# Performance work log

Measured on AMD Instinct MI355X. Metric: run time of the kernel, lower is better.

The kernel has to match this reference:

```python
import jax, jax.numpy as jnp
import numpy as np

COMMITMENT_COST = 0.25


def setup_inputs() -> dict:
    key = jax.random.key(0)
    k1, k2 = jax.random.split(key)
    B, H, W, D, K = 64, 32, 32, 64, 1024
    x = jax.random.normal(k1, (B, H, W, D), dtype=jnp.float32)
    # variance_scaling(fan_in=D, uniform) ~ U(-sqrt(3/D), sqrt(3/D)); plain normal*scale is fine for a reference
    embeddings = jax.random.uniform(k2, (D, K), dtype=jnp.float32,
                                    minval=-np.sqrt(3.0 / D), maxval=np.sqrt(3.0 / D))
    return {"x": x, "embeddings": embeddings}


def reference(x, embeddings):
    D = embeddings.shape[0]
    K = embeddings.shape[1]
    flat = x.reshape(-1, D)                                   # [N, D]
    # squared euclidean distance: ||f||^2 - 2 f.E + ||e||^2 -> [N, K]
    distance = (jnp.sum(flat ** 2, axis=1, keepdims=True)
                - 2.0 * jnp.matmul(flat, embeddings)
                + jnp.sum(embeddings ** 2, axis=0, keepdims=True))
    encoding_indices_flat = jnp.argmax(-distance, axis=1)     # [N]
    encodings = jax.nn.one_hot(encoding_indices_flat, K, dtype=distance.dtype)  # [N, K]
    encoding_indices = encoding_indices_flat.reshape(x.shape[:-1])
    # quantize: gather rows of E^T -> same shape as x
    quantized = jnp.take(embeddings.T, encoding_indices, axis=0)
    e_latent_loss = jnp.mean((jax.lax.stop_gradient(quantized) - x) ** 2)
    q_latent_loss = jnp.mean((quantized - jax.lax.stop_gradient(x)) ** 2)
    loss = q_latent_loss + COMMITMENT_COST * e_latent_loss
    quantized_st = x + jax.lax.stop_gradient(quantized - x)   # straight-through
    avg_probs = jnp.mean(encodings, axis=0)                   # [K]
    perplexity = jnp.exp(-jnp.sum(avg_probs * jnp.log(avg_probs + 1e-10)))
    return quantized_st, loss, perplexity, encoding_indices
```

## Files before the change

### kernel.cpp

```cpp
#include <hip/hip_runtime.h>
#include <math.h>


typedef __attribute__((ext_vector_type(8))) short short8v;
typedef __attribute__((ext_vector_type(4))) float float4v;
typedef unsigned short u16;
typedef unsigned int u32;

constexpr int D = 64;
constexpr int K = 1024;
constexpr int NPTS = 65536;
constexpr long QOFF = (long)NPTS * D;
constexpr float BIAS = 24.0f;
constexpr float GATE = 5e-3f;

constexpr size_t OFF_LOSS = 0;
constexpr size_t OFF_CNT  = 256;
constexpr size_t OFF_EC   = OFF_CNT + 4096;
constexpr size_t OFF_ECB  = OFF_EC + 4096;
constexpr size_t OFF_ET   = OFF_ECB + 4096;
constexpr size_t OFF_STG  = OFF_ET + (size_t)K * D * 4;

__device__ __forceinline__ float med3(float a, float b, float c) {
  return __builtin_amdgcn_fmed3f(a, b, c);
}
__device__ __forceinline__ u16 bf16rtn(float x) {
  u32 u = __float_as_uint(x);
  return (u16)((u + 0x7fffu + ((u >> 16) & 1u)) >> 16);
}
__device__ __forceinline__ float bf2f(u16 h) {
  return __uint_as_float(((u32)h) << 16);
}
__device__ __forceinline__ void gl_lds16(const void* g, void* l) {
  __builtin_amdgcn_global_load_lds(
      (const __attribute__((address_space(1))) u32*)g,
      (__attribute__((address_space(3))) u32*)l, 16, 0, 0);
}

__global__ __launch_bounds__(256) void vq_prep(const float* __restrict__ E,
                                               float* __restrict__ eC,
                                               float* __restrict__ eCb,
                                               float* __restrict__ Et,
                                               unsigned char* __restrict__ stg,
                                               double* __restrict__ lossSum,
                                               int* __restrict__ counts) {
  const int b = blockIdx.x;
  const int tid = threadIdx.x;
  if (b < 32) {
    int gid = b * 256 + tid;
    int k = gid & 1023;
    int g = gid >> 10;
    float v[8];
#pragma unroll
    for (int j = 0; j < 8; ++j) v[j] = E[(g * 8 + j) * K + k];
    *(float4*)&Et[(size_t)k * 64 + g * 8] = make_float4(v[0], v[1], v[2], v[3]);
    *(float4*)&Et[(size_t)k * 64 + g * 8 + 4] = make_float4(v[4], v[5], v[6], v[7]);
    short8v hv, lv;
#pragma unroll
    for (int j = 0; j < 8; ++j) {
      float m2 = -2.0f * v[j];
      u16 h = bf16rtn(m2);
      hv[j] = (short)h;
      lv[j] = (short)bf16rtn(m2 - bf2f(h));
    }
    size_t rowb = (size_t)(k >> 7) * 32768 + (size_t)(k & 127) * 256;
    int s = g >> 2, q = g & 3;
    int off = (s * 64 + q * 16) ^ ((k & 7) * 16);
    *(short8v*)&stg[rowb + off] = hv;
    *(short8v*)&stg[rowb + 128 + off] = lv;
  } else {
    int k = (b - 32) * 256 + tid;
    float c = __fmul_rn(E[k], E[k]);
#pragma unroll
    for (int d = 1; d < D; ++d) {
      float vv = E[d * K + k];
      c = __fadd_rn(c, __fmul_rn(vv, vv));
    }
    eC[k] = c;
    eCb[k] = c + BIAS;
    counts[k] = 0;
    if (k == 0) *lossSum = 0.0;
  }
}

__global__ __launch_bounds__(256) void vq_main(const float* __restrict__ x,
                                               const unsigned char* __restrict__ stg,
                                               const float* __restrict__ eC,
                                               const float* __restrict__ eCb,
                                               const float* __restrict__ Etg,
                                               float* __restrict__ out,
                                               double* __restrict__ lossSum,
                                               int* __restrict__ counts) {
  __shared__ __align__(16) unsigned char sbuf[4][2][8192];
  __shared__ __align__(16) float ecb[1024];
  __shared__ __align__(16) float topbuf[256 * 4];
  __shared__ int bkbuf[128];

  const int tid = threadIdx.x;
  const int w = tid >> 6;
  const int lane = tid & 63;
  const int col = lane & 15;
  const int quad = lane >> 4;
  const int blockBase = blockIdx.x * 128;
  const float INF = __builtin_inff();

  *(float4*)&ecb[tid * 4] = *(const float4*)&eCb[tid * 4];

  short8v Bh[2][2], Bl[2][2];
#pragma unroll
  for (int pt = 0; pt < 2; ++pt) {
    const float* xp = x + (size_t)(blockBase + w * 32 + pt * 16 + col) * 64;
#pragma unroll
    for (int s = 0; s < 2; ++s) {
      const float4* src = (const float4*)(xp + s * 32 + quad * 8);
      float4 a = src[0], b = src[1];
      float xs[8] = {a.x, a.y, a.z, a.w, b.x, b.y, b.z, b.w};
      short8v hf, lf;
#pragma unroll
      for (int j = 0; j < 8; ++j) {
        u16 h = bf16rtn(xs[j]);
        hf[j] = (short)h;
        lf[j] = (short)bf16rtn(xs[j] - bf2f(h));
      }
      Bh[pt][s] = hf;
      Bl[pt][s] = lf;
    }
  }

  {
    const unsigned char* s0 = stg + (size_t)lane * 16;
#pragma unroll
    for (int i = 0; i < 8; ++i)
      gl_lds16(s0 + i * 1024, &sbuf[w][0][i * 1024 + lane * 16]);
#pragma unroll
    for (int i = 0; i < 8; ++i)
      gl_lds16(s0 + 8192 + i * 1024, &sbuf[w][1][i * 1024 + lane * 16]);
  }
  asm volatile("s_waitcnt lgkmcnt(0)" ::: "memory");
  __builtin_amdgcn_s_barrier();
  __builtin_amdgcn_sched_barrier(0);
  asm volatile("" ::: "memory");

  float b1[2] = {INF, INF}, b2[2] = {INF, INF};
  const int swz = (col & 7) * 16;

#pragma unroll 1
  for (int ch = 0; ch < 32; ++ch) {
    const unsigned char* bufB = sbuf[w][ch & 1];
    if (ch < 31) {
      asm volatile("s_waitcnt vmcnt(8)" ::: "memory");
    } else {
      asm volatile("s_waitcnt vmcnt(0)" ::: "memory");
    }
#pragma unroll
    for (int ct2 = 0; ct2 < 2; ++ct2) {
      const int rb = ct2 * 4096 + col * 256;
      short8v Ah0 = *(const short8v*)&bufB[rb + ((quad * 16) ^ swz)];
      short8v Ah1 = *(const short8v*)&bufB[rb + ((64 + quad * 16) ^ swz)];
      short8v Al0 = *(const short8v*)&bufB[rb + 128 + ((quad * 16) ^ swz)];
      short8v Al1 = *(const short8v*)&bufB[rb + 128 + ((64 + quad * 16) ^ swz)];
      float4v Ci = *(const float4v*)&ecb[ch * 32 + ct2 * 16 + quad * 4];
#pragma unroll
      for (int pt = 0; pt < 2; ++pt) {
        float4v Ca = Ci;
        float4v Cb = {0.f, 0.f, 0.f, 0.f};
        Ca = __builtin_amdgcn_mfma_f32_16x16x32_bf16(Ah0, Bh[pt][0], Ca, 0, 0, 0);
        Cb = __builtin_amdgcn_mfma_f32_16x16x32_bf16(Ah1, Bh[pt][1], Cb, 0, 0, 0);
        Ca = __builtin_amdgcn_mfma_f32_16x16x32_bf16(Al0, Bh[pt][0], Ca, 0, 0, 0);
        Cb = __builtin_amdgcn_mfma_f32_16x16x32_bf16(Al1, Bh[pt][1], Cb, 0, 0, 0);
        Ca = __builtin_amdgcn_mfma_f32_16x16x32_bf16(Ah0, Bl[pt][0], Ca, 0, 0, 0);
        Cb = __builtin_amdgcn_mfma_f32_16x16x32_bf16(Ah1, Bl[pt][1], Cb, 0, 0, 0);
#pragma unroll
        for (int r = 0; r < 4; ++r) {
          float dv = Ca[r] + Cb[r];
          u32 u = (__float_as_uint(dv) & 0xffffff00u) |
                  (u32)(ch * 8 + ct2 * 4 + r);
          float v = __uint_as_float(u);
          float pb = b1[pt];
          b1[pt] = fminf(pb, v);
          b2[pt] = med3(pb, b2[pt], v);
        }
      }
    }
    asm volatile("s_waitcnt lgkmcnt(0)" ::: "memory");
    if (ch < 30) {
      const unsigned char* s2 = stg + (size_t)(ch + 2) * 8192 + (size_t)lane * 16;
#pragma unroll
      for (int i = 0; i < 8; ++i)
        gl_lds16(s2 + i * 1024, &sbuf[w][ch & 1][i * 1024 + lane * 16]);
    }
  }

  topbuf[tid * 4 + 0] = b1[0];
  topbuf[tid * 4 + 1] = b2[0];
  topbuf[tid * 4 + 2] = b1[1];
  topbuf[tid * 4 + 3] = b2[1];
  __syncthreads();

  if (tid < 128) {
    const int mw = tid >> 5, mpt = (tid >> 4) & 1, mcol = tid & 15;
    float cv[8];
    int cq[8];
    float mv0 = INF, mv1 = INF;
    int q0 = 0;
#pragma unroll
    for (int q = 0; q < 4; ++q) {
      int lbase = (mw * 64 + q * 16 + mcol) * 4 + mpt * 2;
#pragma unroll
      for (int j = 0; j < 2; ++j) {
        float v = topbuf[lbase + j];
        cv[q * 2 + j] = v;
        cq[q * 2 + j] = q;
        if (v < mv0) { mv1 = mv0; mv0 = v; q0 = q; }
        else if (v < mv1) { mv1 = v; }
      }
    }
    u32 lb = __float_as_uint(mv0) & 255u;
    int bestk = (int)((lb >> 3) * 32 + ((lb >> 2) & 1) * 16 + q0 * 4 + (lb & 3));

    if (mv1 - mv0 < GATE) {
      const float* f = x + (size_t)(blockBase + tid) * 64;
      float r8[8];
#pragma unroll
      for (int j = 0; j < 8; ++j) { float fv = f[j]; r8[j] = __fmul_rn(fv, fv); }
#pragma unroll
      for (int i = 8; i < D; i += 8)
#pragma unroll
        for (int j = 0; j < 8; ++j) {
          float fv = f[i + j];
          r8[j] = __fadd_rn(r8[j], __fmul_rn(fv, fv));
        }
      float A = __fadd_rn(__fadd_rn(__fadd_rn(r8[0], r8[1]), __fadd_rn(r8[2], r8[3])),
                          __fadd_rn(__fadd_rn(r8[4], r8[5]), __fadd_rn(r8[6], r8[7])));
      float bd = INF;
      int bkk = K;
#pragma unroll
      for (int c = 0; c < 8; ++c) {
        u32 cb = __float_as_uint(cv[c]) & 255u;
        int k = (int)((cb >> 3) * 32 + ((cb >> 2) & 1) * 16 + cq[c] * 4 + (cb & 3));
        const float* er = Etg + (size_t)k * 64;
        float m = 0.f;
#pragma unroll
        for (int d = 0; d < D; ++d) m = __fmaf_rn(f[d], er[d], m);
        float dist = __fadd_rn(__fsub_rn(A, __fmul_rn(2.f, m)), eC[k]);
        bool better = (dist < bd) || (dist == bd && k < bkk);
        bd = better ? dist : bd;
        bkk = better ? k : bkk;
      }
      bestk = bkk;
    }

    bkbuf[tid] = bestk;
    out[QOFF + 2 + blockBase + tid] = (float)bestk;
    atomicAdd(&counts[bestk], 1);
  }
  __syncthreads();

  const int pp = tid >> 1, half = tid & 1;
  const int bk = bkbuf[pp];
  const float4* et = (const float4*)(Etg + (size_t)bk * 64 + half * 32);
  const float4* xr = (const float4*)(x + (size_t)(blockBase + pp) * 64 + half * 32);
  float4* ov = (float4*)(out + (size_t)(blockBase + pp) * 64 + half * 32);
  float errs = 0.f;
#pragma unroll
  for (int i = 0; i < 8; ++i) {
    float4 qv = et[i];
    float4 xv = xr[i];
    float dx;
    dx = qv.x - xv.x; errs = fmaf(dx, dx, errs);
    dx = qv.y - xv.y; errs = fmaf(dx, dx, errs);
    dx = qv.z - xv.z; errs = fmaf(dx, dx, errs);
    dx = qv.w - xv.w; errs = fmaf(dx, dx, errs);
    ov[i] = qv;
  }
  double de = (double)errs;
#pragma unroll
  for (int off = 32; off > 0; off >>= 1) de += __shfl_down(de, off, 64);
  if (lane == 0) atomicAdd(lossSum, de);
}

__global__ __launch_bounds__(256) void vq_finalize(const double* __restrict__ lossSum,
                                                   const int* __restrict__ counts,
                                                   float* __restrict__ out) {
  __shared__ double sh[256];
  double ent = 0.0;
  for (int k = threadIdx.x; k < K; k += 256) {
    double pp = (double)counts[k] / (double)NPTS;
    ent += pp * log(pp + 1e-10);
  }
  sh[threadIdx.x] = ent;
  __syncthreads();
  for (int s = 128; s > 0; s >>= 1) {
    if (threadIdx.x < s) sh[threadIdx.x] += sh[threadIdx.x + s];
    __syncthreads();
  }
  if (threadIdx.x == 0) {
    out[QOFF + 0] = (float)(1.25 * (*lossSum) / (double)((long)NPTS * D));
    out[QOFF + 1] = (float)exp(-sh[0]);
  }
}

extern "C" void kernel_launch(void* const* d_in, const int* in_sizes, int n_in,
                              void* d_out, int out_size, void* d_ws, size_t ws_size,
                              hipStream_t stream) {
  const float* x = (const float*)d_in[0];
  const float* E = (const float*)d_in[1];
  float* out = (float*)d_out;

  char* ws = (char*)d_ws;
  double* lossSum = (double*)(ws + OFF_LOSS);
  int* counts = (int*)(ws + OFF_CNT);
  float* eC = (float*)(ws + OFF_EC);
  float* eCb = (float*)(ws + OFF_ECB);
  float* Etg = (float*)(ws + OFF_ET);
  unsigned char* stgb = (unsigned char*)(ws + OFF_STG);

  vq_prep<<<36, 256, 0, stream>>>(E, eC, eCb, Etg, stgb, lossSum, counts);
  vq_main<<<NPTS / 128, 256, 0, stream>>>(x, stgb, eC, eCb, Etg, out,
                                          lossSum, counts);
  vq_finalize<<<1, 256, 0, stream>>>(lossSum, counts, out);
}
```

Measured before the change: 129.4 us.

## Split codebook across waves instead of points, reduce top-2 via shuffles

Each wave now handles all 128 points of the block against a quarter of the codebook (256 codes), not 32 points against all 1024 codes. Each wave streams only its own 8 chunks of staged codebook, and the staging layout is reorganised into MFMA-fragment order so LDS reads are contiguous and unswizzled. The cross-lane top-2 merge now uses xor shuffles and writes into the reused stage buffer, which drops the separate topbuf. In exchange each thread holds 8 point fragments (Bh/Bl[8][2]) and 16 top-2 accumulators, which raises register pressure, and the initial barrier before the loop is removed.

New measurement: 144.5 us. 11.7% more time.

```diff
diff --git a/kernel.cpp b/kernel.cpp
--- a/kernel.cpp
+++ b/kernel.cpp
@@ -63,11 +63,11 @@
       hv[j] = (short)h;
       lv[j] = (short)bf16rtn(m2 - bf2f(h));
     }
-    size_t rowb = (size_t)(k >> 7) * 32768 + (size_t)(k & 127) * 256;
     int s = g >> 2, q = g & 3;
-    int off = (s * 64 + q * 16) ^ ((k & 7) * 16);
-    *(short8v*)&stg[rowb + off] = hv;
-    *(short8v*)&stg[rowb + 128 + off] = lv;
+    size_t tb = (size_t)(k >> 4) * 4096;
+    int lanoff = (q * 16 + (k & 15)) * 16;
+    *(short8v*)&stg[tb + (size_t)s * 1024 + lanoff] = hv;
+    *(short8v*)&stg[tb + (size_t)(2 + s) * 1024 + lanoff] = lv;
   } else {
     int k = (b - 32) * 256 + tid;
     float c = __fmul_rn(E[k], E[k]);
@@ -93,7 +93,6 @@
                                                int* __restrict__ counts) {
   __shared__ __align__(16) unsigned char sbuf[4][2][8192];
   __shared__ __align__(16) float ecb[1024];
-  __shared__ __align__(16) float topbuf[256 * 4];
   __shared__ int bkbuf[128];
 
   const int tid = threadIdx.x;
@@ -106,10 +105,10 @@
 
   *(float4*)&ecb[tid * 4] = *(const float4*)&eCb[tid * 4];
 
-  short8v Bh[2][2], Bl[2][2];
-#pragma unroll
-  for (int pt = 0; pt < 2; ++pt) {
-    const float* xp = x + (size_t)(blockBase + w * 32 + pt * 16 + col) * 64;
+  short8v Bh[8][2], Bl[8][2];
+#pragma unroll
+  for (int pt = 0; pt < 8; ++pt) {
+    const float* xp = x + (size_t)(blockBase + pt * 16 + col) * 64;
 #pragma unroll
     for (int s = 0; s < 2; ++s) {
       const float4* src = (const float4*)(xp + s * 32 + quad * 8);
@@ -128,7 +127,7 @@
   }
 
   {
-    const unsigned char* s0 = stg + (size_t)lane * 16;
+    const unsigned char* s0 = stg + (size_t)(w * 8) * 8192 + (size_t)lane * 16;
 #pragma unroll
     for (int i = 0; i < 8; ++i)
       gl_lds16(s0 + i * 1024, &sbuf[w][0][i * 1024 + lane * 16]);
@@ -136,32 +135,29 @@
     for (int i = 0; i < 8; ++i)
       gl_lds16(s0 + 8192 + i * 1024, &sbuf[w][1][i * 1024 + lane * 16]);
   }
-  asm volatile("s_waitcnt lgkmcnt(0)" ::: "memory");
-  __builtin_amdgcn_s_barrier();
-  __builtin_amdgcn_sched_barrier(0);
-  asm volatile("" ::: "memory");
-
-  float b1[2] = {INF, INF}, b2[2] = {INF, INF};
-  const int swz = (col & 7) * 16;
+
+  float b1[8] = {INF, INF, INF, INF, INF, INF, INF, INF};
+  float b2[8] = {INF, INF, INF, INF, INF, INF, INF, INF};
 
 #pragma unroll 1
-  for (int ch = 0; ch < 32; ++ch) {
+  for (int ch = 0; ch < 8; ++ch) {
     const unsigned char* bufB = sbuf[w][ch & 1];
-    if (ch < 31) {
+    if (ch < 7) {
       asm volatile("s_waitcnt vmcnt(8)" ::: "memory");
     } else {
       asm volatile("s_waitcnt vmcnt(0)" ::: "memory");
     }
 #pragma unroll
     for (int ct2 = 0; ct2 < 2; ++ct2) {
-      const int rb = ct2 * 4096 + col * 256;
-      short8v Ah0 = *(const short8v*)&bufB[rb + ((quad * 16) ^ swz)];
-      short8v Ah1 = *(const short8v*)&bufB[rb + ((64 + quad * 16) ^ swz)];
-      short8v Al0 = *(const short8v*)&bufB[rb + 128 + ((quad * 16) ^ swz)];
-      short8v Al1 = *(const short8v*)&bufB[rb + 128 + ((64 + quad * 16) ^ swz)];
-      float4v Ci = *(const float4v*)&ecb[ch * 32 + ct2 * 16 + quad * 4];
-#pragma unroll
-      for (int pt = 0; pt < 2; ++pt) {
+      const unsigned char* fb = bufB + ct2 * 4096 + lane * 16;
+      short8v Ah0 = *(const short8v*)(fb);
+      short8v Ah1 = *(const short8v*)(fb + 1024);
+      short8v Al0 = *(const short8v*)(fb + 2048);
+      short8v Al1 = *(const short8v*)(fb + 3072);
+      float4v Ci = *(const float4v*)&ecb[w * 256 + ch * 32 + ct2 * 16 + quad * 4];
+      const int idb = ch * 32 + ct2 * 16 + quad * 4;
+#pragma unroll
+      for (int pt = 0; pt < 8; ++pt) {
         float4v Ca = Ci;
         float4v Cb = {0.f, 0.f, 0.f, 0.f};
         Ca = __builtin_amdgcn_mfma_f32_16x16x32_bf16(Ah0, Bh[pt][0], Ca, 0, 0, 0);
@@ -173,8 +169,7 @@
 #pragma unroll
         for (int r = 0; r < 4; ++r) {
           float dv = Ca[r] + Cb[r];
-          u32 u = (__float_as_uint(dv) & 0xffffff00u) |
-                  (u32)(ch * 8 + ct2 * 4 + r);
+          u32 u = (__float_as_uint(dv) & 0xffffff00u) | (u32)(idb + r);
           float v = __uint_as_float(u);
           float pb = b1[pt];
           b1[pt] = fminf(pb, v);
@@ -183,40 +178,54 @@
       }
     }
     asm volatile("s_waitcnt lgkmcnt(0)" ::: "memory");
-    if (ch < 30) {
-      const unsigned char* s2 = stg + (size_t)(ch + 2) * 8192 + (size_t)lane * 16;
+    if (ch < 6) {
+      const unsigned char* s2 =
+          stg + (size_t)(w * 8 + ch + 2) * 8192 + (size_t)lane * 16;
 #pragma unroll
       for (int i = 0; i < 8; ++i)
         gl_lds16(s2 + i * 1024, &sbuf[w][ch & 1][i * 1024 + lane * 16]);
     }
   }
 
-  topbuf[tid * 4 + 0] = b1[0];
-  topbuf[tid * 4 + 1] = b2[0];
-  topbuf[tid * 4 + 2] = b1[1];
-  topbuf[tid * 4 + 3] = b2[1];
+  float* topw = (float*)&sbuf[w][0][0];
+#pragma unroll
+  for (int pt = 0; pt < 8; ++pt) {
+    float v1 = b1[pt], v2 = b2[pt];
+#pragma unroll
+    for (int off = 16; off <= 32; off <<= 1) {
+      float r1 = __shfl_xor(v1, off, 64);
+      float r2 = __shfl_xor(v2, off, 64);
+      float hi = fmaxf(v1, r1);
+      v1 = fminf(v1, r1);
+      v2 = fminf(hi, fminf(v2, r2));
+    }
+    if (lane < 16) {
+      topw[pt * 32 + col * 2] = v1;
+      topw[pt * 32 + col * 2 + 1] = v2;
+    }
+  }
   __syncthreads();
 
   if (tid < 128) {
-    const int mw = tid >> 5, mpt = (tid >> 4) & 1, mcol = tid & 15;
+    const int mpt = tid >> 4, mcol = tid & 15;
     float cv[8];
     int cq[8];
     float mv0 = INF, mv1 = INF;
     int q0 = 0;
 #pragma unroll
-    for (int q = 0; q < 4; ++q) {
-      int lbase = (mw * 64 + q * 16 + mcol) * 4 + mpt * 2;
+    for (int wv = 0; wv < 4; ++wv) {
+      const float* tw = (const float*)&sbuf[wv][0][0];
 #pragma unroll
       for (int j = 0; j < 2; ++j) {
-        float v = topbuf[lbase + j];
-        cv[q * 2 + j] = v;
-        cq[q * 2 + j] = q;
-        if (v < mv0) { mv1 = mv0; mv0 = v; q0 = q; }
+        float v = tw[mpt * 32 + mcol * 2 + j];
+        cv[wv * 2 + j] = v;
+        cq[wv * 2 + j] = wv;
+        if (v < mv0) { mv1 = mv0; mv0 = v; q0 = wv; }
         else if (v < mv1) { mv1 = v; }
       }
     }
     u32 lb = __float_as_uint(mv0) & 255u;
-    int bestk = (int)((lb >> 3) * 32 + ((lb >> 2) & 1) * 16 + q0 * 4 + (lb & 3));
+    int bestk = q0 * 256 + (int)lb;
 
     if (mv1 - mv0 < GATE) {
       const float* f = x + (size_t)(blockBase + tid) * 64;
@@ -236,8 +245,7 @@
       int bkk = K;
 #pragma unroll
       for (int c = 0; c < 8; ++c) {
-        u32 cb = __float_as_uint(cv[c]) & 255u;
-        int k = (int)((cb >> 3) * 32 + ((cb >> 2) & 1) * 16 + cq[c] * 4 + (cb & 3));
+        int k = cq[c] * 256 + (int)(__float_as_uint(cv[c]) & 255u);
         const float* er = Etg + (size_t)k * 64;
         float m = 0.f;
 #pragma unroll
```

## Fuse finalize into main kernel via last-block counter and pre-fragment codebook layout

Applied to the files above, without the earlier changes.

Removes the separate finalize launch. A global done counter lets the last-finishing block of vq_main compute the perplexity and loss outputs. The staged bf16 codebook is also rearranged into MFMA fragment order, so each lane reads contiguous 16-byte chunks at lane*16 with no XOR swizzle arithmetic. The trade-off is an extra atomic and barrier per block, and the fused epilogue depends on relaxed atomics being visible across blocks.

After: 135.7 us. 1.05x slower.

```diff
diff --git a/kernel.cpp b/kernel.cpp
--- a/kernel.cpp
+++ b/kernel.cpp
@@ -15,6 +15,7 @@
 constexpr float GATE = 5e-3f;
 
 constexpr size_t OFF_LOSS = 0;
+constexpr size_t OFF_DONE = 16;
 constexpr size_t OFF_CNT  = 256;
 constexpr size_t OFF_EC   = OFF_CNT + 4096;
 constexpr size_t OFF_ECB  = OFF_EC + 4096;
@@ -43,7 +44,8 @@
                                                float* __restrict__ Et,
                                                unsigned char* __restrict__ stg,
                                                double* __restrict__ lossSum,
-                                               int* __restrict__ counts) {
+                                               int* __restrict__ counts,
+                                               int* __restrict__ done) {
   const int b = blockIdx.x;
   const int tid = threadIdx.x;
   if (b < 32) {
@@ -63,11 +65,11 @@
       hv[j] = (short)h;
       lv[j] = (short)bf16rtn(m2 - bf2f(h));
     }
-    size_t rowb = (size_t)(k >> 7) * 32768 + (size_t)(k & 127) * 256;
     int s = g >> 2, q = g & 3;
-    int off = (s * 64 + q * 16) ^ ((k & 7) * 16);
-    *(short8v*)&stg[rowb + off] = hv;
-    *(short8v*)&stg[rowb + 128 + off] = lv;
+    size_t tb = (size_t)(k >> 4) * 4096;
+    int lanoff = (q * 16 + (k & 15)) * 16;
+    *(short8v*)&stg[tb + (size_t)s * 1024 + lanoff] = hv;
+    *(short8v*)&stg[tb + (size_t)(2 + s) * 1024 + lanoff] = lv;
   } else {
     int k = (b - 32) * 256 + tid;
     float c = __fmul_rn(E[k], E[k]);
@@ -79,7 +81,7 @@
     eC[k] = c;
     eCb[k] = c + BIAS;
     counts[k] = 0;
-    if (k == 0) *lossSum = 0.0;
+    if (k == 0) { *lossSum = 0.0; *done = 0; }
   }
 }
 
@@ -90,11 +92,13 @@
                                                const float* __restrict__ Etg,
                                                float* __restrict__ out,
                                                double* __restrict__ lossSum,
-                                               int* __restrict__ counts) {
+                                               int* __restrict__ counts,
+                                               int* __restrict__ done) {
   __shared__ __align__(16) unsigned char sbuf[4][2][8192];
   __shared__ __align__(16) float ecb[1024];
   __shared__ __align__(16) float topbuf[256 * 4];
   __shared__ int bkbuf[128];
+  __shared__ int lastFlag;
 
   const int tid = threadIdx.x;
   const int w = tid >> 6;
@@ -142,7 +146,6 @@
   asm volatile("" ::: "memory");
 
   float b1[2] = {INF, INF}, b2[2] = {INF, INF};
-  const int swz = (col & 7) * 16;
 
 #pragma unroll 1
   for (int ch = 0; ch < 32; ++ch) {
@@ -154,11 +157,11 @@
     }
 #pragma unroll
     for (int ct2 = 0; ct2 < 2; ++ct2) {
-      const int rb = ct2 * 4096 + col * 256;
-      short8v Ah0 = *(const short8v*)&bufB[rb + ((quad * 16) ^ swz)];
-      short8v Ah1 = *(const short8v*)&bufB[rb + ((64 + quad * 16) ^ swz)];
-      short8v Al0 = *(const short8v*)&bufB[rb + 128 + ((quad * 16) ^ swz)];
-      short8v Al1 = *(const short8v*)&bufB[rb + 128 + ((64 + quad * 16) ^ swz)];
+      const unsigned char* fb = bufB + ct2 * 4096 + lane * 16;
+      short8v Ah0 = *(const short8v*)(fb);
+      short8v Ah1 = *(const short8v*)(fb + 1024);
+      short8v Al0 = *(const short8v*)(fb + 2048);
+      short8v Al1 = *(const short8v*)(fb + 3072);
       float4v Ci = *(const float4v*)&ecb[ch * 32 + ct2 * 16 + quad * 4];
 #pragma unroll
       for (int pt = 0; pt < 2; ++pt) {
@@ -277,26 +280,37 @@
 #pragma unroll
   for (int off = 32; off > 0; off >>= 1) de += __shfl_down(de, off, 64);
   if (lane == 0) atomicAdd(lossSum, de);
-}
-
-__global__ __launch_bounds__(256) void vq_finalize(const double* __restrict__ lossSum,
-                                                   const int* __restrict__ counts,
-                                                   float* __restrict__ out) {
-  __shared__ double sh[256];
-  double ent = 0.0;
-  for (int k = threadIdx.x; k < K; k += 256) {
-    double pp = (double)counts[k] / (double)NPTS;
-    ent += pp * log(pp + 1e-10);
-  }
-  sh[threadIdx.x] = ent;
+
   __syncthreads();
-  for (int s = 128; s > 0; s >>= 1) {
-    if (threadIdx.x < s) sh[threadIdx.x] += sh[threadIdx.x + s];
+  if (tid == 0) {
+    int t = __hip_atomic_fetch_add(done, 1, __ATOMIC_RELAXED,
+                                   __HIP_MEMORY_SCOPE_AGENT);
+    lastFlag = (t == (int)gridDim.x - 1);
+  }
+  __syncthreads();
+  if (lastFlag) {
+    double ent = 0.0;
+    for (int k = tid; k < K; k += 256) {
+      int c = __hip_atomic_load(&counts[k], __ATOMIC_RELAXED,
+                                __HIP_MEMORY_SCOPE_AGENT);
+      double pp2 = (double)c / (double)NPTS;
+      ent += pp2 * log(pp2 + 1e-10);
+    }
+    double* sh = (double*)topbuf;
+    sh[tid] = ent;
     __syncthreads();
-  }
-  if (threadIdx.x == 0) {
-    out[QOFF + 0] = (float)(1.25 * (*lossSum) / (double)((long)NPTS * D));
-    out[QOFF + 1] = (float)exp(-sh[0]);
+    for (int s = 128; s > 0; s >>= 1) {
+      if (tid < s) sh[tid] += sh[tid + s];
+      __syncthreads();
+    }
+    if (tid == 0) {
+      unsigned long long lb = __hip_atomic_load((const unsigned long long*)lossSum,
+                                                __ATOMIC_RELAXED,
+                                                __HIP_MEMORY_SCOPE_AGENT);
+      double L = __longlong_as_double(lb);
+      out[QOFF + 0] = (float)(1.25 * L / (double)((long)NPTS * D));
+      out[QOFF + 1] = (float)exp(-sh[0]);
+    }
   }
 }
 
@@ -309,14 +323,14 @@
 
   char* ws = (char*)d_ws;
   double* lossSum = (double*)(ws + OFF_LOSS);
+  int* done = (int*)(ws + OFF_DONE);
   int* counts = (int*)(ws + OFF_CNT);
   float* eC = (float*)(ws + OFF_EC);
   float* eCb = (float*)(ws + OFF_ECB);
   float* Etg = (float*)(ws + OFF_ET);
   unsigned char* stgb = (unsigned char*)(ws + OFF_STG);
 
-  vq_prep<<<36, 256, 0, stream>>>(E, eC, eCb, Etg, stgb, lossSum, counts);
+  vq_prep<<<36, 256, 0, stream>>>(E, eC, eCb, Etg, stgb, lossSum, counts, done);
   vq_main<<<NPTS / 128, 256, 0, stream>>>(x, stgb, eC, eCb, Etg, out,
-                                          lossSum, counts);
-  vq_finalize<<<1, 256, 0, stream>>>(lossSum, counts, out);
-}
+                                          lossSum, counts, done);
+}
```
